# Optimization experiments

Hardware: AMD Instinct MI355X
Metric: run time of the kernel (lower is better)

The kernel has to match this reference:

```python
import jax, jax.numpy as jnp
import numpy as np

N = 50000      # nodes
E = 600000     # edges
F_IN = 128     # num_node_features
H = 128        # hidden_channels
C = 10         # num_classes
G = 128        # graphs in batch


def setup_inputs() -> dict:
    key = jax.random.key(0)
    ks = jax.random.split(key, 12)
    x = jax.random.normal(ks[0], (N, F_IN), dtype=jnp.float32)
    edge_index = jax.random.randint(ks[1], (2, E), 0, N, dtype=jnp.int64)
    batch = jnp.sort(jax.random.randint(ks[2], (N,), 0, G, dtype=jnp.int64))
    s = 0.05
    return {
        "x": x,
        "W1": jax.random.normal(ks[3], (F_IN, H), jnp.float32) * s,
        "b1": jnp.zeros((H,), jnp.float32),
        "W2": jax.random.normal(ks[4], (H, H), jnp.float32) * s,
        "b2": jnp.zeros((H,), jnp.float32),
        "W3": jax.random.normal(ks[5], (H, H), jnp.float32) * s,
        "b3": jnp.zeros((H,), jnp.float32),
        "Wl": jax.random.normal(ks[6], (H, C), jnp.float32) * s,
        "bl": jnp.zeros((C,), jnp.float32),
        "edge_index": edge_index,
        "batch": batch,
    }


def _gcn_conv(h, W, b, src, dst, norm, n):
    # h: [N, din] -> linear (no bias), gather, scale, scatter-add, + bias
    h = h @ W                                  # [N, dout]
    msg = norm[:, None] * h[src]               # [E+N, dout]
    out = jax.ops.segment_sum(msg, dst, num_segments=n)
    return out + b


def reference(x, W1, b1, W2, b2, W3, b3, Wl, bl, edge_index, batch):
    n = x.shape[0]
    # add self-loops (PyG GCNConv default) and symmetric normalization
    loop = jnp.arange(n, dtype=edge_index.dtype)
    src = jnp.concatenate([edge_index[0], loop])   # [E+N]
    dst = jnp.concatenate([edge_index[1], loop])   # [E+N]
    deg = jax.ops.segment_sum(jnp.ones_like(dst, dtype=x.dtype), dst, num_segments=n)
    dinv = jnp.where(deg > 0, jax.lax.rsqrt(deg), 0.0)
    norm = dinv[src] * dinv[dst]                   # [E+N]

    h = jax.nn.relu(_gcn_conv(x, W1, b1, src, dst, norm, n))
    h = jax.nn.relu(_gcn_conv(h, W2, b2, src, dst, norm, n))
    h = jax.nn.relu(_gcn_conv(h, W3, b3, src, dst, norm, n))

    # global mean pool over graph ids
    sums = jax.ops.segment_sum(h, batch, num_segments=G)           # [G, H]
    cnts = jax.ops.segment_sum(jnp.ones((n,), h.dtype), batch, num_segments=G)
    pooled = sums / jnp.maximum(cnts, 1.0)[:, None]

    # dropout is identity at inference; final linear classifier
    return pooled @ Wl + bl                                        # [G, C]
```

## Files before the change

kernel.cpp:

```cpp
#include <hip/hip_runtime.h>

#define HID 128
#define CLS 10
#define RCAP 64

typedef short short8 __attribute__((ext_vector_type(8)));
typedef float f32x4 __attribute__((ext_vector_type(4)));

__device__ __forceinline__ unsigned short f2bf(float f) {
  union { float f; unsigned u; } v; v.f = f;
  unsigned u = v.u;
  return (unsigned short)((u + 0x7FFFu + ((u >> 16) & 1u)) >> 16);
}
__device__ __forceinline__ float bf_lo(unsigned p) { return __uint_as_float(p << 16); }
__device__ __forceinline__ float bf_hi(unsigned p) { return __uint_as_float(p & 0xFFFF0000u); }


__global__ __launch_bounds__(256) void zero_wt(int* __restrict__ degi, int n, int nbN,
                                               float* __restrict__ pooled, int gh,
                                               const float* __restrict__ W1,
                                               const float* __restrict__ W2,
                                               const float* __restrict__ W3,
                                               unsigned short* __restrict__ Wt) {
  int b = blockIdx.x;
  if (b < nbN) {
    int i = b * 256 + threadIdx.x;
    if (i < n) degi[i] = 0;
    if (i < gh) pooled[i] = 0.f;
    return;
  }
  int wb = b - nbN;
  int mat = wb >> 4;
  int part = wb & 15;
  const float* W = (mat == 0) ? W1 : (mat == 1) ? W2 : W3;
  unsigned short* o = Wt + (size_t)mat * HID * HID;
  int base = part * (HID * HID / 16);
  for (int r = 0; r < HID * HID / 16; r += 256) {
    int idx = base + r + threadIdx.x;
    int k = idx >> 7, nn = idx & 127;
    o[nn * HID + k] = f2bf(W[idx]);
  }
}

__global__ __launch_bounds__(256) void degree_fill(const int* __restrict__ src,
                                                   const int* __restrict__ dst,
                                                   int* __restrict__ degi,
                                                   int* __restrict__ col_src, int E) {
  int e = blockIdx.x * 256 + threadIdx.x;
  if (e >= E) return;
  int d = dst[e];
  int slot = atomicAdd(&degi[d], 1);
  if (slot < RCAP) col_src[(size_t)d * RCAP + slot] = src[e];
}


#define WTP 136

__global__ __launch_bounds__(256) void gemm_mfma(const void* __restrict__ Aptr,
                                                 int a_fp32,
                                                 const unsigned short* __restrict__ Wt,
                                                 const int* __restrict__ degi,
                                                 unsigned short* __restrict__ Tb,
                                                 int nrows) {
  __shared__ unsigned short sW[HID][WTP];
  int tid = threadIdx.x;
  int wave = tid >> 6, lane = tid & 63;
  int m_lo = lane & 15, quad = lane >> 4;
  int row0 = blockIdx.x * 128;
  int rbase = row0 + wave * 32;

  uint4 araw[2][4];
#pragma unroll
  for (int tr = 0; tr < 2; ++tr) {
    int grow = rbase + tr * 16 + m_lo;
    int gr = (grow < nrows) ? grow : (nrows - 1);
    if (a_fp32) {
      const float* Arow = (const float*)Aptr + (size_t)gr * HID;
#pragma unroll
      for (int kb = 0; kb < 4; ++kb) {
        float4 f0 = *(const float4*)&Arow[kb * 32 + quad * 8];
        float4 f1 = *(const float4*)&Arow[kb * 32 + quad * 8 + 4];
        uint4 u;
        u.x = (unsigned)f2bf(f0.x) | ((unsigned)f2bf(f0.y) << 16);
        u.y = (unsigned)f2bf(f0.z) | ((unsigned)f2bf(f0.w) << 16);
        u.z = (unsigned)f2bf(f1.x) | ((unsigned)f2bf(f1.y) << 16);
        u.w = (unsigned)f2bf(f1.z) | ((unsigned)f2bf(f1.w) << 16);
        araw[tr][kb] = u;
      }
    } else {
      const uint4* Arow = (const uint4*)((const unsigned*)Aptr + (size_t)gr * 64);
#pragma unroll
      for (int kb = 0; kb < 4; ++kb) araw[tr][kb] = Arow[kb * 4 + quad];
    }
  }

  const uint4* Wt4 = (const uint4*)Wt;
#pragma unroll
  for (int i = 0; i < 8; ++i) {
    int idx = i * 256 + tid;
    *(uint4*)&sW[idx >> 4][(idx & 15) * 8] = Wt4[idx];
  }
  __syncthreads();

  f32x4 acc[2][8];
#pragma unroll
  for (int tr = 0; tr < 2; ++tr)
#pragma unroll
    for (int tc = 0; tc < 8; ++tc) acc[tr][tc] = (f32x4)(0.f);

#pragma unroll
  for (int kb = 0; kb < 4; ++kb) {
    short8 b[8];
#pragma unroll
    for (int tc = 0; tc < 8; ++tc) {
      union { uint4 u; short8 s; } cv;
      cv.u = *(const uint4*)&sW[tc * 16 + m_lo][kb * 32 + quad * 8];
      b[tc] = cv.s;
    }
#pragma unroll
    for (int tr = 0; tr < 2; ++tr) {
      union { uint4 u; short8 s; } av;
      av.u = araw[tr][kb];
#pragma unroll
      for (int tc = 0; tc < 8; ++tc)
        acc[tr][tc] = __builtin_amdgcn_mfma_f32_16x16x32_bf16(av.s, b[tc], acc[tr][tc], 0, 0, 0);
    }
  }

#pragma unroll
  for (int tr = 0; tr < 2; ++tr) {
#pragma unroll
    for (int r = 0; r < 4; ++r) {
      int grow = rbase + tr * 16 + quad * 4 + r;
      if (grow < nrows) {
        float s = rsqrtf((float)degi[grow] + 1.0f);
        unsigned short* orow = &Tb[(size_t)grow * HID];
#pragma unroll
        for (int tc = 0; tc < 8; ++tc)
          orow[tc * 16 + m_lo] = f2bf(s * acc[tr][tc][r]);
      }
    }
  }
}


__device__ __forceinline__ void agg_node(const unsigned* __restrict__ Tb2,
                                         const int* __restrict__ degi,
                                         const int* __restrict__ col_src,
                                         const float* __restrict__ bias,
                                         int node, int l4, float a[8]) {
  uint4 sv = *(const uint4*)&Tb2[(size_t)node * 64 + l4 * 4];
  a[0] = bf_lo(sv.x); a[1] = bf_hi(sv.x); a[2] = bf_lo(sv.y); a[3] = bf_hi(sv.y);
  a[4] = bf_lo(sv.z); a[5] = bf_hi(sv.z); a[6] = bf_lo(sv.w); a[7] = bf_hi(sv.w);
  int deg = degi[node];
  const int* row = &col_src[(size_t)node * RCAP];
  int j = 0;
  for (; j + 8 <= deg; j += 8) {
    int idx[8];
#pragma unroll
    for (int u = 0; u < 8; ++u) idx[u] = row[j + u];
    uint4 v[8];
#pragma unroll
    for (int u = 0; u < 8; ++u) v[u] = *(const uint4*)&Tb2[(size_t)idx[u] * 64 + l4 * 4];
#pragma unroll
    for (int u = 0; u < 8; ++u) {
      a[0] += bf_lo(v[u].x); a[1] += bf_hi(v[u].x);
      a[2] += bf_lo(v[u].y); a[3] += bf_hi(v[u].y);
      a[4] += bf_lo(v[u].z); a[5] += bf_hi(v[u].z);
      a[6] += bf_lo(v[u].w); a[7] += bf_hi(v[u].w);
    }
  }
  if (j + 4 <= deg) {
    int idx[4];
#pragma unroll
    for (int u = 0; u < 4; ++u) idx[u] = row[j + u];
    uint4 v[4];
#pragma unroll
    for (int u = 0; u < 4; ++u) v[u] = *(const uint4*)&Tb2[(size_t)idx[u] * 64 + l4 * 4];
#pragma unroll
    for (int u = 0; u < 4; ++u) {
      a[0] += bf_lo(v[u].x); a[1] += bf_hi(v[u].x);
      a[2] += bf_lo(v[u].y); a[3] += bf_hi(v[u].y);
      a[4] += bf_lo(v[u].z); a[5] += bf_hi(v[u].z);
      a[6] += bf_lo(v[u].w); a[7] += bf_hi(v[u].w);
    }
    j += 4;
  }
  for (; j < deg; ++j) {
    uint4 v = *(const uint4*)&Tb2[(size_t)row[j] * 64 + l4 * 4];
    a[0] += bf_lo(v.x); a[1] += bf_hi(v.x);
    a[2] += bf_lo(v.y); a[3] += bf_hi(v.y);
    a[4] += bf_lo(v.z); a[5] += bf_hi(v.z);
    a[6] += bf_lo(v.w); a[7] += bf_hi(v.w);
  }
  float di = rsqrtf((float)deg + 1.0f);
  float4 bs0 = *(const float4*)&bias[l4 * 8];
  float4 bs1 = *(const float4*)&bias[l4 * 8 + 4];
  a[0] = fmaxf(di * a[0] + bs0.x, 0.f);
  a[1] = fmaxf(di * a[1] + bs0.y, 0.f);
  a[2] = fmaxf(di * a[2] + bs0.z, 0.f);
  a[3] = fmaxf(di * a[3] + bs0.w, 0.f);
  a[4] = fmaxf(di * a[4] + bs1.x, 0.f);
  a[5] = fmaxf(di * a[5] + bs1.y, 0.f);
  a[6] = fmaxf(di * a[6] + bs1.z, 0.f);
  a[7] = fmaxf(di * a[7] + bs1.w, 0.f);
}

__global__ __launch_bounds__(256) void aggregate(const unsigned* __restrict__ Tb2,
                                                 const int* __restrict__ degi,
                                                 const int* __restrict__ col_src,
                                                 const float* __restrict__ bias,
                                                 unsigned* __restrict__ Hb, int n) {
  int w = (blockIdx.x * 256 + threadIdx.x) >> 6;
  int lane = threadIdx.x & 63;
  int sub = lane >> 4;
  int l4 = lane & 15;
  int node = w * 4 + sub;
  if (node >= n) return;
  float a[8];
  agg_node(Tb2, degi, col_src, bias, node, l4, a);
  uint4 o;
  o.x = (unsigned)f2bf(a[0]) | ((unsigned)f2bf(a[1]) << 16);
  o.y = (unsigned)f2bf(a[2]) | ((unsigned)f2bf(a[3]) << 16);
  o.z = (unsigned)f2bf(a[4]) | ((unsigned)f2bf(a[5]) << 16);
  o.w = (unsigned)f2bf(a[6]) | ((unsigned)f2bf(a[7]) << 16);
  *(uint4*)&Hb[(size_t)node * 64 + l4 * 4] = o;
}

#define SPP 132

__global__ __launch_bounds__(256) void aggregate_pool(const unsigned* __restrict__ Tb2,
                                                      const int* __restrict__ degi,
                                                      const int* __restrict__ col_src,
                                                      const float* __restrict__ bias,
                                                      const int* __restrict__ batch,
                                                      float* __restrict__ pooled, int n) {
  __shared__ float sP[16][SPP];
  int tid = threadIdx.x;
  int wave = tid >> 6, lane = tid & 63;
  int sub = lane >> 4;
  int l4 = lane & 15;
  int base = blockIdx.x * 16;
  int nl = wave * 4 + sub;
  int node = base + nl;
  bool active = (node < n);

  float a[8] = {0.f, 0.f, 0.f, 0.f, 0.f, 0.f, 0.f, 0.f};
  if (active) agg_node(Tb2, degi, col_src, bias, node, l4, a);
  *(float4*)&sP[nl][l4 * 8] = make_float4(a[0], a[1], a[2], a[3]);
  *(float4*)&sP[nl][l4 * 8 + 4] = make_float4(a[4], a[5], a[6], a[7]);
  __syncthreads();

  if (tid < HID) {
    int g = -1;
    float acc = 0.f;
    for (int i = 0; i < 16; ++i) {
      int nd = base + i;
      if (nd >= n) break;
      int bi = batch[nd];
      if (bi != g) {
        if (g >= 0) atomicAdd(&pooled[g * HID + tid], acc);
        acc = 0.f;
        g = bi;
      }
      acc += sP[i][tid];
    }
    if (g >= 0) atomicAdd(&pooled[g * HID + tid], acc);
  }
}

__global__ __launch_bounds__(128) void classify_k(const float* __restrict__ pooled,
                                                  const int* __restrict__ batch,
                                                  const float* __restrict__ Wl,
                                                  const float* __restrict__ bl,
                                                  float* __restrict__ out, int n) {
  int g = blockIdx.x;
  int t = threadIdx.x;
  int lo = 0, hi = n;
  while (lo < hi) { int mid = (lo + hi) >> 1; if (batch[mid] < g) lo = mid + 1; else hi = mid; }
  int s = lo;
  hi = n;
  while (lo < hi) { int mid = (lo + hi) >> 1; if (batch[mid] < g + 1) lo = mid + 1; else hi = mid; }
  float c = fmaxf((float)(lo - s), 1.0f);
  __shared__ float p[HID];
  p[t] = pooled[g * HID + t] / c;
  __syncthreads();
  if (t < CLS) {
    float o = bl[t];
    for (int j = 0; j < HID; ++j) o += p[j] * Wl[j * CLS + t];
    out[g * CLS + t] = o;
  }
}


extern "C" void kernel_launch(void* const* d_in, const int* in_sizes, int n_in,
                              void* d_out, int out_size, void* d_ws, size_t ws_size,
                              hipStream_t stream) {
  const float* x  = (const float*)d_in[0];
  const float* W1 = (const float*)d_in[1];
  const float* b1 = (const float*)d_in[2];
  const float* W2 = (const float*)d_in[3];
  const float* b2 = (const float*)d_in[4];
  const float* W3 = (const float*)d_in[5];
  const float* b3 = (const float*)d_in[6];
  const float* Wl = (const float*)d_in[7];
  const float* bl = (const float*)d_in[8];
  const int* edge_index = (const int*)d_in[9];
  const int* batch = (const int*)d_in[10];

  const int N = in_sizes[10];
  const int E = in_sizes[9] / 2;
  const int G = out_size / CLS;
  const int* src = edge_index;
  const int* dst = edge_index + E;

  uintptr_t p = (uintptr_t)d_ws;
  auto take = [&](size_t bytes) -> void* {
    void* r = (void*)p;
    p += (bytes + 255) & ~(size_t)255;
    return r;
  };
  int*      degi      = (int*)take((size_t)N * 4);
  int*      col_src   = (int*)take((size_t)N * RCAP * 4);
  unsigned short* WtA = (unsigned short*)take((size_t)3 * HID * HID * 2);
  unsigned short* bufTb = (unsigned short*)take((size_t)N * HID * 2);
  unsigned* bufHb     = (unsigned*)take((size_t)N * 64 * 4);
  float*    pooled    = (float*)take((size_t)G * HID * 4);

  int nbN = (N + 255) / 256;
  int nbE = (E + 255) / 256;

  zero_wt<<<nbN + 48, 256, 0, stream>>>(degi, N, nbN, pooled, G * HID, W1, W2, W3, WtA);
  degree_fill<<<nbE, 256, 0, stream>>>(src, dst, degi, col_src, E);

  int gemmBlocks = (N + 127) / 128;
  int waves = (N + 3) / 4;
  int aggBlocks = (waves + 3) / 4;

  gemm_mfma<<<gemmBlocks, 256, 0, stream>>>(x, 1, WtA, degi, bufTb, N);
  aggregate<<<aggBlocks, 256, 0, stream>>>((unsigned*)bufTb, degi, col_src, b1, bufHb, N);
  gemm_mfma<<<gemmBlocks, 256, 0, stream>>>(bufHb, 0, WtA + (size_t)HID * HID, degi, bufTb, N);
  aggregate<<<aggBlocks, 256, 0, stream>>>((unsigned*)bufTb, degi, col_src, b2, bufHb, N);
  gemm_mfma<<<gemmBlocks, 256, 0, stream>>>(bufHb, 0, WtA + (size_t)2 * HID * HID, degi, bufTb, N);
  aggregate_pool<<<(N + 15) / 16, 256, 0, stream>>>((unsigned*)bufTb, degi, col_src, b3,
                                                    batch, pooled, N);
  classify_k<<<G, 128, 0, stream>>>(pooled, batch, Wl, bl, (float*)d_out, N);
}
```

Before: 250.1 us.

## Aggregate each node with a full wave, splitting neighbors across sub-groups

Each GCN aggregation node now gets a full 64-lane wave instead of a 16-lane quarter. The four 16-lane sub-groups each take every fourth neighbor and combine their partial sums with cross-lane shuffles. The aim is more memory-level parallelism per node and less imbalance from degree variance within a wave. The cost is four times as many waves, extra shuffle work, and only a quarter of the lanes doing the final store. The pooling kernel moves to 1024-thread blocks so it still covers 16 nodes per block.

```diff
diff --git a/kernel.cpp b/kernel.cpp
--- a/kernel.cpp
+++ b/kernel.cpp
@@ -144,54 +144,43 @@
 }
 
 
-__device__ __forceinline__ void agg_node(const unsigned* __restrict__ Tb2,
-                                         const int* __restrict__ degi,
-                                         const int* __restrict__ col_src,
-                                         const float* __restrict__ bias,
-                                         int node, int l4, float a[8]) {
-  uint4 sv = *(const uint4*)&Tb2[(size_t)node * 64 + l4 * 4];
-  a[0] = bf_lo(sv.x); a[1] = bf_hi(sv.x); a[2] = bf_lo(sv.y); a[3] = bf_hi(sv.y);
-  a[4] = bf_lo(sv.z); a[5] = bf_hi(sv.z); a[6] = bf_lo(sv.w); a[7] = bf_hi(sv.w);
+__device__ __forceinline__ void accum_row(float a[8], uint4 v) {
+  a[0] += bf_lo(v.x); a[1] += bf_hi(v.x);
+  a[2] += bf_lo(v.y); a[3] += bf_hi(v.y);
+  a[4] += bf_lo(v.z); a[5] += bf_hi(v.z);
+  a[6] += bf_lo(v.w); a[7] += bf_hi(v.w);
+}
+
+__device__ __forceinline__ void agg_node_wave(const unsigned* __restrict__ Tb2,
+                                              const int* __restrict__ degi,
+                                              const int* __restrict__ col_src,
+                                              const float* __restrict__ bias,
+                                              int node, int sub, int l4, float a[8]) {
+#pragma unroll
+  for (int k = 0; k < 8; ++k) a[k] = 0.f;
   int deg = degi[node];
   const int* row = &col_src[(size_t)node * RCAP];
-  int j = 0;
-  for (; j + 8 <= deg; j += 8) {
-    int idx[8];
-#pragma unroll
-    for (int u = 0; u < 8; ++u) idx[u] = row[j + u];
-    uint4 v[8];
-#pragma unroll
-    for (int u = 0; u < 8; ++u) v[u] = *(const uint4*)&Tb2[(size_t)idx[u] * 64 + l4 * 4];
-#pragma unroll
-    for (int u = 0; u < 8; ++u) {
-      a[0] += bf_lo(v[u].x); a[1] += bf_hi(v[u].x);
-      a[2] += bf_lo(v[u].y); a[3] += bf_hi(v[u].y);
-      a[4] += bf_lo(v[u].z); a[5] += bf_hi(v[u].z);
-      a[6] += bf_lo(v[u].w); a[7] += bf_hi(v[u].w);
-    }
-  }
-  if (j + 4 <= deg) {
-    int idx[4];
-#pragma unroll
-    for (int u = 0; u < 4; ++u) idx[u] = row[j + u];
-    uint4 v[4];
-#pragma unroll
-    for (int u = 0; u < 4; ++u) v[u] = *(const uint4*)&Tb2[(size_t)idx[u] * 64 + l4 * 4];
-#pragma unroll
-    for (int u = 0; u < 4; ++u) {
-      a[0] += bf_lo(v[u].x); a[1] += bf_hi(v[u].x);
-      a[2] += bf_lo(v[u].y); a[3] += bf_hi(v[u].y);
-      a[4] += bf_lo(v[u].z); a[5] += bf_hi(v[u].z);
-      a[6] += bf_lo(v[u].w); a[7] += bf_hi(v[u].w);
-    }
-    j += 4;
-  }
-  for (; j < deg; ++j) {
+  if (sub == 0) {
+    uint4 sv = *(const uint4*)&Tb2[(size_t)node * 64 + l4 * 4];
+    accum_row(a, sv);
+  }
+  int j = sub;
+  for (; j + 4 < deg; j += 8) {
+    int i0 = row[j];
+    int i1 = row[j + 4];
+    uint4 v0 = *(const uint4*)&Tb2[(size_t)i0 * 64 + l4 * 4];
+    uint4 v1 = *(const uint4*)&Tb2[(size_t)i1 * 64 + l4 * 4];
+    accum_row(a, v0);
+    accum_row(a, v1);
+  }
+  if (j < deg) {
     uint4 v = *(const uint4*)&Tb2[(size_t)row[j] * 64 + l4 * 4];
-    a[0] += bf_lo(v.x); a[1] += bf_hi(v.x);
-    a[2] += bf_lo(v.y); a[3] += bf_hi(v.y);
-    a[4] += bf_lo(v.z); a[5] += bf_hi(v.z);
-    a[6] += bf_lo(v.w); a[7] += bf_hi(v.w);
+    accum_row(a, v);
+  }
+#pragma unroll
+  for (int k = 0; k < 8; ++k) {
+    a[k] += __shfl_xor(a[k], 16, 64);
+    a[k] += __shfl_xor(a[k], 32, 64);
   }
   float di = rsqrtf((float)deg + 1.0f);
   float4 bs0 = *(const float4*)&bias[l4 * 8];
@@ -211,44 +200,48 @@
                                                  const int* __restrict__ col_src,
                                                  const float* __restrict__ bias,
                                                  unsigned* __restrict__ Hb, int n) {
-  int w = (blockIdx.x * 256 + threadIdx.x) >> 6;
+  int wave = threadIdx.x >> 6;
   int lane = threadIdx.x & 63;
   int sub = lane >> 4;
   int l4 = lane & 15;
-  int node = w * 4 + sub;
+  int node = blockIdx.x * 4 + wave;
   if (node >= n) return;
   float a[8];
-  agg_node(Tb2, degi, col_src, bias, node, l4, a);
-  uint4 o;
-  o.x = (unsigned)f2bf(a[0]) | ((unsigned)f2bf(a[1]) << 16);
-  o.y = (unsigned)f2bf(a[2]) | ((unsigned)f2bf(a[3]) << 16);
-  o.z = (unsigned)f2bf(a[4]) | ((unsigned)f2bf(a[5]) << 16);
-  o.w = (unsigned)f2bf(a[6]) | ((unsigned)f2bf(a[7]) << 16);
-  *(uint4*)&Hb[(size_t)node * 64 + l4 * 4] = o;
+  agg_node_wave(Tb2, degi, col_src, bias, node, sub, l4, a);
+  if (sub == 0) {
+    uint4 o;
+    o.x = (unsigned)f2bf(a[0]) | ((unsigned)f2bf(a[1]) << 16);
+    o.y = (unsigned)f2bf(a[2]) | ((unsigned)f2bf(a[3]) << 16);
+    o.z = (unsigned)f2bf(a[4]) | ((unsigned)f2bf(a[5]) << 16);
+    o.w = (unsigned)f2bf(a[6]) | ((unsigned)f2bf(a[7]) << 16);
+    *(uint4*)&Hb[(size_t)node * 64 + l4 * 4] = o;
+  }
 }
 
 #define SPP 132
 
-__global__ __launch_bounds__(256) void aggregate_pool(const unsigned* __restrict__ Tb2,
-                                                      const int* __restrict__ degi,
-                                                      const int* __restrict__ col_src,
-                                                      const float* __restrict__ bias,
-                                                      const int* __restrict__ batch,
-                                                      float* __restrict__ pooled, int n) {
+__global__ __launch_bounds__(1024) void aggregate_pool(const unsigned* __restrict__ Tb2,
+                                                       const int* __restrict__ degi,
+                                                       const int* __restrict__ col_src,
+                                                       const float* __restrict__ bias,
+                                                       const int* __restrict__ batch,
+                                                       float* __restrict__ pooled, int n) {
   __shared__ float sP[16][SPP];
   int tid = threadIdx.x;
   int wave = tid >> 6, lane = tid & 63;
   int sub = lane >> 4;
   int l4 = lane & 15;
   int base = blockIdx.x * 16;
-  int nl = wave * 4 + sub;
-  int node = base + nl;
-  bool active = (node < n);
-
-  float a[8] = {0.f, 0.f, 0.f, 0.f, 0.f, 0.f, 0.f, 0.f};
-  if (active) agg_node(Tb2, degi, col_src, bias, node, l4, a);
-  *(float4*)&sP[nl][l4 * 8] = make_float4(a[0], a[1], a[2], a[3]);
-  *(float4*)&sP[nl][l4 * 8 + 4] = make_float4(a[4], a[5], a[6], a[7]);
+  int node = base + wave;
+
+  if (node < n) {
+    float a[8];
+    agg_node_wave(Tb2, degi, col_src, bias, node, sub, l4, a);
+    if (sub == 0) {
+      *(float4*)&sP[wave][l4 * 8] = make_float4(a[0], a[1], a[2], a[3]);
+      *(float4*)&sP[wave][l4 * 8 + 4] = make_float4(a[4], a[5], a[6], a[7]);
+    }
+  }
   __syncthreads();
 
   if (tid < HID) {
@@ -334,15 +327,15 @@
   degree_fill<<<nbE, 256, 0, stream>>>(src, dst, degi, col_src, E);
 
   int gemmBlocks = (N + 127) / 128;
-  int waves = (N + 3) / 4;
-  int aggBlocks = (waves + 3) / 4;
+  int aggBlocks = (N + 3) / 4;
+  int poolBlocks = (N + 15) / 16;
 
   gemm_mfma<<<gemmBlocks, 256, 0, stream>>>(x, 1, WtA, degi, bufTb, N);
   aggregate<<<aggBlocks, 256, 0, stream>>>((unsigned*)bufTb, degi, col_src, b1, bufHb, N);
   gemm_mfma<<<gemmBlocks, 256, 0, stream>>>(bufHb, 0, WtA + (size_t)HID * HID, degi, bufTb, N);
   aggregate<<<aggBlocks, 256, 0, stream>>>((unsigned*)bufTb, degi, col_src, b2, bufHb, N);
   gemm_mfma<<<gemmBlocks, 256, 0, stream>>>(bufHb, 0, WtA + (size_t)2 * HID * HID, degi, bufTb, N);
-  aggregate_pool<<<(N + 15) / 16, 256, 0, stream>>>((unsigned*)bufTb, degi, col_src, b3,
-                                                    batch, pooled, N);
+  aggregate_pool<<<poolBlocks, 1024, 0, stream>>>((unsigned*)bufTb, degi, col_src, b3,
+                                                  batch, pooled, N);
   classify_k<<<G, 128, 0, stream>>>(pooled, batch, Wl, bl, (float*)d_out, N);
 }
```

Result: slower. 263.4 us (+5.3%).
